# Performance work log

Measured on AMD Instinct MI355X. Metric: run time of the kernel, lower is better.

## Reference

```python
import jax, jax.numpy as jnp
import numpy as np

LEN_M = 131328   # (data_dim+1) * d_h = 513 * 256
D_H = 256
N_MC = 64
DATA_DIM_P1 = 513
N = 4096


def setup_inputs() -> dict:
    key = jax.random.key(0)
    k1, k2, k3, k4 = jax.random.split(key, 4)
    params = jax.random.normal(k1, (2 * LEN_M,), dtype=jnp.float32)
    W1 = jax.random.normal(k2, (D_H + 1,), dtype=jnp.float32)
    x = jax.random.normal(k3, (N, DATA_DIM_P1), dtype=jnp.float32)
    eps = jax.random.normal(k4, (N_MC,), dtype=jnp.float32)
    return {"params": params, "W1": W1, "x": x, "eps": eps}


def reference(params, W1, x, eps):
    # split variational params into means and (relu'd) variances
    m_w0 = params[:LEN_M]                                  # [len_m]
    v_w0 = jax.nn.relu(params[LEN_M:]) + 1e-6              # [len_m]
    # reparameterized MC sampling; NOTE: torch code draws ONE scalar eps per
    # MC sample (randn(m_w0[0].shape) is scalar), shared across all weights.
    samps_w0 = m_w0[:, None] + eps[None, :] * jnp.sqrt(v_w0)[:, None]  # [len_m, M]
    W0 = samps_w0.reshape(DATA_DIM_P1, D_H, N_MC)          # [d+1, h, M]
    # fused batched GEMM replacing the d_h * num_MC_samps tiny matmuls
    x_w0 = jnp.einsum('nd,dhm->nhm', x, W0)                # [N, h, M]
    z = jax.nn.relu(x_w0)
    ones = jnp.ones((x.shape[0], 1, N_MC), dtype=x.dtype)
    z = jnp.concatenate([ones, z], axis=1)                 # [N, h+1, M]
    pred_samps = jnp.einsum('nhm,h->nm', z, W1)            # [N, M]
    return pred_samps, m_w0, v_w0
```

## Files before the change

kernel.cpp:

```cpp
#include <hip/hip_runtime.h>
#include <hip/hip_bf16.h>
#include <math.h>

#define LEN_M   131328
#define D_P1    513
#define NROW    4096
#define PRED_ELEMS (NROW * 64)

typedef __attribute__((ext_vector_type(8))) short short8;
typedef __attribute__((ext_vector_type(4))) float floatx4;
typedef __attribute__((ext_vector_type(2))) float v2f;

__device__ __forceinline__ void gl_lds16(const void* g, void* l)
{
    __builtin_amdgcn_global_load_lds(
        (const __attribute__((address_space(1))) unsigned int*)g,
        (__attribute__((address_space(3))) unsigned int*)l, 16, 0, 0);
}

__device__ __forceinline__ unsigned short bf16b(float f)
{
    __hip_bfloat16 h = __float2bfloat16(f);
    return *(unsigned short*)&h;
}

__global__ __launch_bounds__(256) void prep_kernel(
    const float* __restrict__ params, float* __restrict__ out,
    __hip_bfloat16* __restrict__ wcbt)
{
    __shared__ unsigned short T[64][65];
    const int bid = blockIdx.x;
    const int t   = threadIdx.x;

    if (bid < 1024) {
        int i = bid * 256 + t;
        out[i] = 0.0f;
        if (i < LEN_M) {
            float m = params[i];
            float v = fmaxf(params[LEN_M + i], 0.0f) + 1e-6f;
            out[PRED_ELEMS + i]         = m;
            out[PRED_ELEMS + LEN_M + i] = v;
        }
        return;
    }

    const int b2 = bid - 1024;
    const int k0 = (b2 & 7) * 64;
    const int c0 = (b2 >> 3) * 64;
    const int hh = t & 63, kb = t >> 6;
    const bool spart = (c0 >= 256);
    const int hbase = c0 & 255;
    const float* src = params + (spart ? LEN_M : 0);

    #pragma unroll 4
    for (int p = 0; p < 16; ++p) {
        int kk = p * 4 + kb;
        float v = src[(k0 + kk) * 256 + hbase + hh];
        if (spart) v = sqrtf(fmaxf(v, 0.0f) + 1e-6f);
        T[kk][hh] = bf16b(v);
    }
    __syncthreads();

    const int cc = t >> 2, kq = t & 3;
    short8 lo, hi;
    #pragma unroll
    for (int j = 0; j < 8; ++j) lo[j] = (short)T[kq * 16 + j][cc];
    #pragma unroll
    for (int j = 0; j < 8; ++j) hi[j] = (short)T[kq * 16 + 8 + j][cc];

    const int cR  = c0 + cc;
    const int swz = (cR >> 1) & 3;
    const int g1  = (k0 >> 3) + 2 * kq;
    const int g2  = g1 + 1;
    const int d1  = cR * 64 + (g1 & ~3) + ((g1 & 3) ^ swz);
    const int d2  = cR * 64 + (g2 & ~3) + ((g2 & 3) ^ swz);
    short* wb = (short*)wcbt;
    *(short8*)(wb + d1 * 8) = lo;
    *(short8*)(wb + d2 * 8) = hi;
}

__global__ __launch_bounds__(256) void main_kernel(
    const __hip_bfloat16* __restrict__ wcbt, const float* __restrict__ params,
    const float* __restrict__ x, const float* __restrict__ W1,
    const float* __restrict__ eps, float* __restrict__ out)
{
    __shared__ char smem[128 * 36 * 4];
    short* Bs   = (short*)smem;
    short* As   = (short*)(smem + 8192);
    float* Clds = (float*)smem;

    const int t = threadIdx.x;
    const int w4 = t >> 6, lane = t & 63;
    const int lane15 = lane & 15, quad = lane >> 4;
    const int H  = blockIdx.x;
    const int bm = blockIdx.y * 32;

    const short* wb = (const short*)wcbt;
    const short* bsrc0; const short* bsrc1; short* bdst0; short* bdst1;
    {
        int ch0 = t, ch1 = 256 + t;
        int lc0 = ch0 >> 2, qs0 = ch0 & 3;
        int lc1 = ch1 >> 2, qs1 = ch1 & 3;
        int c0g = H * 64 + lc0 + ((lc0 >> 6) * 192);
        int c1g = H * 64 + lc1 + ((lc1 >> 6) * 192);
        bsrc0 = wb + (c0g * 64 + qs0) * 8;
        bsrc1 = wb + (c1g * 64 + qs1) * 8;
        bdst0 = Bs + ch0 * 8;
        bdst1 = Bs + ch1 * 8;
    }

    const int ar = t >> 3, asub = t & 7;
    const int aq = asub >> 1, ahalf = asub & 1;
    const float* axp = x + (bm + ar) * D_P1 + asub * 4;
    unsigned short* adst = (unsigned short*)As + ar * 32
                         + ((aq ^ ((ar >> 1) & 3)) * 8) + ahalf * 4;

    const float e = eps[lane];
    float xl[2][4];
    #pragma unroll
    for (int rh = 0; rh < 2; ++rh)
        #pragma unroll
        for (int i = 0; i < 4; ++i)
            xl[rh][i] = x[(bm + rh * 16 + quad * 4 + i) * D_P1 + 512];
    float wl[2];
    #pragma unroll
    for (int s = 0; s < 2; ++s) {
        int lc = w4 * 32 + s * 16 + lane15;
        int c  = H * 64 + lc + ((lc >> 6) * 192);
        wl[s] = (c < 256) ? params[131072 + c]
                          : sqrtf(fmaxf(params[LEN_M + 131072 + (c - 256)], 0.0f) + 1e-6f);
    }

    const short* afp[2]; const short* bfp[2];
    #pragma unroll
    for (int rh = 0; rh < 2; ++rh) {
        int row = rh * 16 + lane15;
        afp[rh] = As + row * 32 + ((quad ^ ((row >> 1) & 3)) * 8);
    }
    #pragma unroll
    for (int s = 0; s < 2; ++s) {
        int lc = w4 * 32 + s * 16 + lane15;
        bfp[s] = Bs + lc * 32 + ((quad ^ ((lc >> 1) & 3)) * 8);
    }

    floatx4 acc00 = {0.f,0.f,0.f,0.f}, acc01 = acc00, acc10 = acc00, acc11 = acc00;

    for (int ks = 0; ks < 16; ++ks) {
        gl_lds16(bsrc0 + ks * 32, bdst0);
        gl_lds16(bsrc1 + ks * 32, bdst1);
        float f0 = axp[ks * 32 + 0], f1 = axp[ks * 32 + 1];
        float f2 = axp[ks * 32 + 2], f3 = axp[ks * 32 + 3];
        ushort4 pk;
        pk.x = bf16b(f0); pk.y = bf16b(f1); pk.z = bf16b(f2); pk.w = bf16b(f3);
        *(ushort4*)adst = pk;
        __syncthreads();

        short8 a0 = *(const short8*)afp[0];
        short8 a1 = *(const short8*)afp[1];
        short8 b0 = *(const short8*)bfp[0];
        short8 b1 = *(const short8*)bfp[1];
        acc00 = __builtin_amdgcn_mfma_f32_16x16x32_bf16(a0, b0, acc00, 0, 0, 0);
        acc01 = __builtin_amdgcn_mfma_f32_16x16x32_bf16(a0, b1, acc01, 0, 0, 0);
        acc10 = __builtin_amdgcn_mfma_f32_16x16x32_bf16(a1, b0, acc10, 0, 0, 0);
        acc11 = __builtin_amdgcn_mfma_f32_16x16x32_bf16(a1, b1, acc11, 0, 0, 0);
        __syncthreads();
    }

    floatx4 accs[2][2] = {{acc00, acc01}, {acc10, acc11}};
    #pragma unroll
    for (int rh = 0; rh < 2; ++rh)
        #pragma unroll
        for (int s = 0; s < 2; ++s) {
            float4 o;
            o.x = accs[rh][s][0] + xl[rh][0] * wl[s];
            o.y = accs[rh][s][1] + xl[rh][1] * wl[s];
            o.z = accs[rh][s][2] + xl[rh][2] * wl[s];
            o.w = accs[rh][s][3] + xl[rh][3] * wl[s];
            int lc = w4 * 32 + s * 16 + lane15;
            int r0 = rh * 16 + quad * 4;
            *(float4*)&Clds[lc * 36 + r0] = o;
        }
    __syncthreads();

    const int rb = w4 * 8;
    const float binit = (H == 0) ? W1[0] : 0.0f;
    v2f accp[4];
    #pragma unroll
    for (int j = 0; j < 4; ++j) accp[j] = (v2f){binit, binit};
    const v2f e2 = {e, e};
    const v2f z2 = {0.f, 0.f};

    #pragma unroll 4
    for (int lh = 0; lh < 64; ++lh) {
        const float w1h = W1[1 + H * 64 + lh];
        const v2f w2 = {w1h, w1h};
        const v2f* ap = (const v2f*)&Clds[lh * 36 + rb];
        const v2f* bp = (const v2f*)&Clds[(64 + lh) * 36 + rb];
        #pragma unroll
        for (int j = 0; j < 4; ++j) {
            v2f t2 = __builtin_elementwise_fma(e2, bp[j], ap[j]);
            t2 = __builtin_elementwise_max(t2, z2);
            accp[j] = __builtin_elementwise_fma(t2, w2, accp[j]);
        }
    }

    float* op = out + (bm + rb) * 64 + lane;
    #pragma unroll
    for (int j = 0; j < 4; ++j) {
        unsafeAtomicAdd(op + (2 * j) * 64,     accp[j].x);
        unsafeAtomicAdd(op + (2 * j + 1) * 64, accp[j].y);
    }
}

extern "C" void kernel_launch(void* const* d_in, const int* in_sizes, int n_in,
                              void* d_out, int out_size, void* d_ws, size_t ws_size,
                              hipStream_t stream)
{
    const float* params = (const float*)d_in[0];
    const float* W1     = (const float*)d_in[1];
    const float* x      = (const float*)d_in[2];
    const float* eps    = (const float*)d_in[3];
    float* out = (float*)d_out;
    __hip_bfloat16* wcbt = (__hip_bfloat16*)d_ws;

    prep_kernel<<<1024 + 64, 256, 0, stream>>>(params, out, wcbt);
    main_kernel<<<dim3(4, 128), 256, 0, stream>>>(wcbt, params, x, W1, eps, out);
}
```

Before: 85.21 us.

## Stage full A tile in LDS upfront and double-buffer B loads

The main kernel now converts and stores the whole 32x512 bf16 A tile into LDS once before the K loop, using a new XOR swizzle. It also double-buffers the B tile so the global-to-LDS load for the next K step is issued while the current step's MFMAs run. This drops one barrier per iteration and overlaps global latency with compute. In exchange LDS use grows to 48 KB, and the last iteration prefetches one step past the tile, reading into the next column or possibly past the workspace end.

Result: no change. 84.83 us (-0.5%).

```diff
diff --git a/kernel.cpp b/kernel.cpp
--- a/kernel.cpp
+++ b/kernel.cpp
@@ -84,10 +84,10 @@
     const float* __restrict__ x, const float* __restrict__ W1,
     const float* __restrict__ eps, float* __restrict__ out)
 {
-    __shared__ char smem[128 * 36 * 4];
-    short* Bs   = (short*)smem;
-    short* As   = (short*)(smem + 8192);
-    float* Clds = (float*)smem;
+    __shared__ char smem[49152];
+    char*  Bs   = smem;
+    char*  As   = smem + 16384;
+    float* Clds = (float*)(smem + 16384);
 
     const int t = threadIdx.x;
     const int w4 = t >> 6, lane = t & 63;
@@ -96,7 +96,7 @@
     const int bm = blockIdx.y * 32;
 
     const short* wb = (const short*)wcbt;
-    const short* bsrc0; const short* bsrc1; short* bdst0; short* bdst1;
+    const short* bsrc0; const short* bsrc1;
     {
         int ch0 = t, ch1 = 256 + t;
         int lc0 = ch0 >> 2, qs0 = ch0 & 3;
@@ -105,15 +105,29 @@
         int c1g = H * 64 + lc1 + ((lc1 >> 6) * 192);
         bsrc0 = wb + (c0g * 64 + qs0) * 8;
         bsrc1 = wb + (c1g * 64 + qs1) * 8;
-        bdst0 = Bs + ch0 * 8;
-        bdst1 = Bs + ch1 * 8;
-    }
-
-    const int ar = t >> 3, asub = t & 7;
-    const int aq = asub >> 1, ahalf = asub & 1;
-    const float* axp = x + (bm + ar) * D_P1 + asub * 4;
-    unsigned short* adst = (unsigned short*)As + ar * 32
-                         + ((aq ^ ((ar >> 1) & 3)) * 8) + ahalf * 4;
+    }
+    char* bd0 = Bs + t * 16;
+    char* bd1 = Bs + 4096 + t * 16;
+
+    gl_lds16(bsrc0, bd0);
+    gl_lds16(bsrc1, bd1);
+
+    {
+        const int ar = t >> 3, a8 = t & 7;
+        const float* axp = x + (bm + ar) * D_P1;
+        unsigned short* arow = (unsigned short*)As + ar * 512;
+        #pragma unroll 4
+        for (int ks = 0; ks < 16; ++ks) {
+            int k = ks * 32 + a8 * 4;
+            float f0 = axp[k], f1 = axp[k + 1], f2 = axp[k + 2], f3 = axp[k + 3];
+            int chunk = k >> 3;
+            int half  = a8 & 1;
+            int cs = (chunk & ~7) | ((chunk & 7) ^ (ar & 7));
+            ushort4 pk;
+            pk.x = bf16b(f0); pk.y = bf16b(f1); pk.z = bf16b(f2); pk.w = bf16b(f3);
+            *(ushort4*)(arow + cs * 8 + half * 4) = pk;
+        }
+    }
 
     const float e = eps[lane];
     float xl[2][4];
@@ -131,34 +145,30 @@
                           : sqrtf(fmaxf(params[LEN_M + 131072 + (c - 256)], 0.0f) + 1e-6f);
     }
 
-    const short* afp[2]; const short* bfp[2];
-    #pragma unroll
-    for (int rh = 0; rh < 2; ++rh) {
-        int row = rh * 16 + lane15;
-        afp[rh] = As + row * 32 + ((quad ^ ((row >> 1) & 3)) * 8);
-    }
+    int bfo[2];
     #pragma unroll
     for (int s = 0; s < 2; ++s) {
         int lc = w4 * 32 + s * 16 + lane15;
-        bfp[s] = Bs + lc * 32 + ((quad ^ ((lc >> 1) & 3)) * 8);
-    }
+        bfo[s] = lc * 64 + ((quad ^ ((lc >> 1) & 3)) * 16);
+    }
+    const int ax7 = lane15 & 7;
 
     floatx4 acc00 = {0.f,0.f,0.f,0.f}, acc01 = acc00, acc10 = acc00, acc11 = acc00;
 
+    __syncthreads();
+
     for (int ks = 0; ks < 16; ++ks) {
-        gl_lds16(bsrc0 + ks * 32, bdst0);
-        gl_lds16(bsrc1 + ks * 32, bdst1);
-        float f0 = axp[ks * 32 + 0], f1 = axp[ks * 32 + 1];
-        float f2 = axp[ks * 32 + 2], f3 = axp[ks * 32 + 3];
-        ushort4 pk;
-        pk.x = bf16b(f0); pk.y = bf16b(f1); pk.z = bf16b(f2); pk.w = bf16b(f3);
-        *(ushort4*)adst = pk;
-        __syncthreads();
-
-        short8 a0 = *(const short8*)afp[0];
-        short8 a1 = *(const short8*)afp[1];
-        short8 b0 = *(const short8*)bfp[0];
-        short8 b1 = *(const short8*)bfp[1];
+        const int nb = (ks + 1) & 1;
+        gl_lds16(bsrc0 + (ks + 1) * 32, bd0 + nb * 8192);
+        gl_lds16(bsrc1 + (ks + 1) * 32, bd1 + nb * 8192);
+
+        const int cs16 = ((ks >> 1) * 8 + (((ks & 1) * 4 + quad) ^ ax7)) * 16;
+        short8 a0 = *(const short8*)(As + lane15 * 1024 + cs16);
+        short8 a1 = *(const short8*)(As + (16 + lane15) * 1024 + cs16);
+        const char* Bb = Bs + (ks & 1) * 8192;
+        short8 b0 = *(const short8*)(Bb + bfo[0]);
+        short8 b1 = *(const short8*)(Bb + bfo[1]);
+
         acc00 = __builtin_amdgcn_mfma_f32_16x16x32_bf16(a0, b0, acc00, 0, 0, 0);
         acc01 = __builtin_amdgcn_mfma_f32_16x16x32_bf16(a0, b1, acc01, 0, 0, 0);
         acc10 = __builtin_amdgcn_mfma_f32_16x16x32_bf16(a1, b0, acc10, 0, 0, 0);
```

## Restructure main GEMM to full-width 512-column tiles with double-buffered LDS

Applied to the files above, without the earlier changes.

Each block now owns 16 rows and all 512 weight columns (means and std parts), so the ReLU/W1 reduction finishes inside the block. This removes the atomic adds and the zeroing of the prediction output. The weight workspace layout changes to k-chunk-major with an XOR swizzle, so whole 64-deep k-chunks stream into LDS through double buffering. The bf16 row of x is converted once up front. The cost is 144KB of dynamic LDS per block, which limits occupancy to one block per CU with only 256 blocks.

New measurement: 84.43 us. No clear change (-0.9%).

```diff
diff --git a/kernel.cpp b/kernel.cpp
--- a/kernel.cpp
+++ b/kernel.cpp
@@ -32,19 +32,16 @@
     const int bid = blockIdx.x;
     const int t   = threadIdx.x;
 
-    if (bid < 1024) {
+    if (bid < 513) {
         int i = bid * 256 + t;
-        out[i] = 0.0f;
-        if (i < LEN_M) {
-            float m = params[i];
-            float v = fmaxf(params[LEN_M + i], 0.0f) + 1e-6f;
-            out[PRED_ELEMS + i]         = m;
-            out[PRED_ELEMS + LEN_M + i] = v;
-        }
+        float m = params[i];
+        float v = fmaxf(params[LEN_M + i], 0.0f) + 1e-6f;
+        out[PRED_ELEMS + i]         = m;
+        out[PRED_ELEMS + LEN_M + i] = v;
         return;
     }
 
-    const int b2 = bid - 1024;
+    const int b2 = bid - 513;
     const int k0 = (b2 & 7) * 64;
     const int c0 = (b2 >> 3) * 64;
     const int hh = t & 63, kb = t >> 6;
@@ -68,147 +65,148 @@
     #pragma unroll
     for (int j = 0; j < 8; ++j) hi[j] = (short)T[kq * 16 + 8 + j][cc];
 
-    const int cR  = c0 + cc;
-    const int swz = (cR >> 1) & 3;
-    const int g1  = (k0 >> 3) + 2 * kq;
-    const int g2  = g1 + 1;
-    const int d1  = cR * 64 + (g1 & ~3) + ((g1 & 3) ^ swz);
-    const int d2  = cR * 64 + (g2 & ~3) + ((g2 & 3) ^ swz);
+    const int cR = c0 + cc;
+    const int g1 = (k0 >> 3) + 2 * kq;
+    const int g2 = g1 + 1;
+    const int d1 = (g1 >> 3) * 4096 + cR * 8 + ((g1 & 7) ^ (cR & 7));
+    const int d2 = (g2 >> 3) * 4096 + cR * 8 + ((g2 & 7) ^ (cR & 7));
     short* wb = (short*)wcbt;
     *(short8*)(wb + d1 * 8) = lo;
     *(short8*)(wb + d2 * 8) = hi;
 }
 
-__global__ __launch_bounds__(256) void main_kernel(
+__global__ __launch_bounds__(512) void main_kernel(
     const __hip_bfloat16* __restrict__ wcbt, const float* __restrict__ params,
     const float* __restrict__ x, const float* __restrict__ W1,
     const float* __restrict__ eps, float* __restrict__ out)
 {
-    __shared__ char smem[128 * 36 * 4];
-    short* Bs   = (short*)smem;
-    short* As   = (short*)(smem + 8192);
-    float* Clds = (float*)smem;
+    extern __shared__ char smem[];
+    char*  Ap = smem + 131072;
+    float* Cl = (float*)smem;
+    float* P  = (float*)(smem + 40960);
 
     const int t = threadIdx.x;
-    const int w4 = t >> 6, lane = t & 63;
+    const int w = t >> 6, lane = t & 63;
     const int lane15 = lane & 15, quad = lane >> 4;
-    const int H  = blockIdx.x;
-    const int bm = blockIdx.y * 32;
-
-    const short* wb = (const short*)wcbt;
-    const short* bsrc0; const short* bsrc1; short* bdst0; short* bdst1;
+    const int ax7 = lane15 & 7;
+    const int bm = blockIdx.x * 16;
+
+    const char* wbase = (const char*)wcbt;
+
+    #pragma unroll
+    for (int i = 0; i < 8; ++i)
+        gl_lds16(wbase + (0 * 4096 + i * 512 + t) * 16, smem + i * 8192 + t * 16);
+
     {
-        int ch0 = t, ch1 = 256 + t;
-        int lc0 = ch0 >> 2, qs0 = ch0 & 3;
-        int lc1 = ch1 >> 2, qs1 = ch1 & 3;
-        int c0g = H * 64 + lc0 + ((lc0 >> 6) * 192);
-        int c1g = H * 64 + lc1 + ((lc1 >> 6) * 192);
-        bsrc0 = wb + (c0g * 64 + qs0) * 8;
-        bsrc1 = wb + (c1g * 64 + qs1) * 8;
-        bdst0 = Bs + ch0 * 8;
-        bdst1 = Bs + ch1 * 8;
-    }
-
-    const int ar = t >> 3, asub = t & 7;
-    const int aq = asub >> 1, ahalf = asub & 1;
-    const float* axp = x + (bm + ar) * D_P1 + asub * 4;
-    unsigned short* adst = (unsigned short*)As + ar * 32
-                         + ((aq ^ ((ar >> 1) & 3)) * 8) + ahalf * 4;
+        const int r = t >> 5, seg = t & 31;
+        const float* xrow = x + (bm + r) * D_P1 + seg * 16;
+        #pragma unroll
+        for (int c2 = 0; c2 < 2; ++c2) {
+            int g  = seg * 2 + c2;
+            int cs = (g & ~7) | ((g & 7) ^ (r & 7));
+            short8 pk;
+            #pragma unroll
+            for (int j = 0; j < 8; ++j) pk[j] = (short)bf16b(xrow[c2 * 8 + j]);
+            *(short8*)(Ap + r * 1024 + cs * 16) = pk;
+        }
+    }
 
     const float e = eps[lane];
-    float xl[2][4];
-    #pragma unroll
-    for (int rh = 0; rh < 2; ++rh)
-        #pragma unroll
-        for (int i = 0; i < 4; ++i)
-            xl[rh][i] = x[(bm + rh * 16 + quad * 4 + i) * D_P1 + 512];
-    float wl[2];
-    #pragma unroll
-    for (int s = 0; s < 2; ++s) {
-        int lc = w4 * 32 + s * 16 + lane15;
-        int c  = H * 64 + lc + ((lc >> 6) * 192);
+    float xl[4];
+    #pragma unroll
+    for (int i = 0; i < 4; ++i)
+        xl[i] = x[(bm + quad * 4 + i) * D_P1 + 512];
+    float wl[4];
+    #pragma unroll
+    for (int s = 0; s < 4; ++s) {
+        int c = (s < 2 ? 0 : 256) + w * 32 + (s & 1) * 16 + lane15;
         wl[s] = (c < 256) ? params[131072 + c]
                           : sqrtf(fmaxf(params[LEN_M + 131072 + (c - 256)], 0.0f) + 1e-6f);
     }
 
-    const short* afp[2]; const short* bfp[2];
-    #pragma unroll
-    for (int rh = 0; rh < 2; ++rh) {
-        int row = rh * 16 + lane15;
-        afp[rh] = As + row * 32 + ((quad ^ ((row >> 1) & 3)) * 8);
-    }
-    #pragma unroll
-    for (int s = 0; s < 2; ++s) {
-        int lc = w4 * 32 + s * 16 + lane15;
-        bfp[s] = Bs + lc * 32 + ((quad ^ ((lc >> 1) & 3)) * 8);
-    }
-
-    floatx4 acc00 = {0.f,0.f,0.f,0.f}, acc01 = acc00, acc10 = acc00, acc11 = acc00;
-
-    for (int ks = 0; ks < 16; ++ks) {
-        gl_lds16(bsrc0 + ks * 32, bdst0);
-        gl_lds16(bsrc1 + ks * 32, bdst1);
-        float f0 = axp[ks * 32 + 0], f1 = axp[ks * 32 + 1];
-        float f2 = axp[ks * 32 + 2], f3 = axp[ks * 32 + 3];
-        ushort4 pk;
-        pk.x = bf16b(f0); pk.y = bf16b(f1); pk.z = bf16b(f2); pk.w = bf16b(f3);
-        *(ushort4*)adst = pk;
+    int cb[4];
+    #pragma unroll
+    for (int s = 0; s < 4; ++s)
+        cb[s] = ((s < 2 ? 0 : 256) + w * 32 + (s & 1) * 16 + lane15) * 128;
+
+    floatx4 acc[4];
+    #pragma unroll
+    for (int s = 0; s < 4; ++s) acc[s] = (floatx4){0.f, 0.f, 0.f, 0.f};
+
+    __syncthreads();
+
+    for (int kc = 0; kc < 8; ++kc) {
+        if (kc < 7) {
+            const int nb = (kc + 1) & 1;
+            #pragma unroll
+            for (int i = 0; i < 8; ++i)
+                gl_lds16(wbase + ((kc + 1) * 4096 + i * 512 + t) * 16,
+                         smem + nb * 65536 + i * 8192 + t * 16);
+        }
+        const char* Bb = smem + (kc & 1) * 65536;
+        const char* Ab = Ap + lane15 * 1024 + kc * 128;
+        #pragma unroll
+        for (int kk = 0; kk < 2; ++kk) {
+            const int off = ((kk * 4 + quad) ^ ax7) * 16;
+            short8 a  = *(const short8*)(Ab + off);
+            short8 b0 = *(const short8*)(Bb + cb[0] + off);
+            short8 b1 = *(const short8*)(Bb + cb[1] + off);
+            short8 b2 = *(const short8*)(Bb + cb[2] + off);
+            short8 b3 = *(const short8*)(Bb + cb[3] + off);
+            acc[0] = __builtin_amdgcn_mfma_f32_16x16x32_bf16(a, b0, acc[0], 0, 0, 0);
+            acc[1] = __builtin_amdgcn_mfma_f32_16x16x32_bf16(a, b1, acc[1], 0, 0, 0);
+            acc[2] = __builtin_amdgcn_mfma_f32_16x16x32_bf16(a, b2, acc[2], 0, 0, 0);
+            acc[3] = __builtin_amdgcn_mfma_f32_16x16x32_bf16(a, b3, acc[3], 0, 0, 0);
+        }
         __syncthreads();
-
-        short8 a0 = *(const short8*)afp[0];
-        short8 a1 = *(const short8*)afp[1];
-        short8 b0 = *(const short8*)bfp[0];
-        short8 b1 = *(const short8*)bfp[1];
-        acc00 = __builtin_amdgcn_mfma_f32_16x16x32_bf16(a0, b0, acc00, 0, 0, 0);
-        acc01 = __builtin_amdgcn_mfma_f32_16x16x32_bf16(a0, b1, acc01, 0, 0, 0);
-        acc10 = __builtin_amdgcn_mfma_f32_16x16x32_bf16(a1, b0, acc10, 0, 0, 0);
-        acc11 = __builtin_amdgcn_mfma_f32_16x16x32_bf16(a1, b1, acc11, 0, 0, 0);
-        __syncthreads();
-    }
-
-    floatx4 accs[2][2] = {{acc00, acc01}, {acc10, acc11}};
-    #pragma unroll
-    for (int rh = 0; rh < 2; ++rh)
-        #pragma unroll
-        for (int s = 0; s < 2; ++s) {
-            float4 o;
-            o.x = accs[rh][s][0] + xl[rh][0] * wl[s];
-            o.y = accs[rh][s][1] + xl[rh][1] * wl[s];
-            o.z = accs[rh][s][2] + xl[rh][2] * wl[s];
-            o.w = accs[rh][s][3] + xl[rh][3] * wl[s];
-            int lc = w4 * 32 + s * 16 + lane15;
-            int r0 = rh * 16 + quad * 4;
-            *(float4*)&Clds[lc * 36 + r0] = o;
-        }
-    __syncthreads();
-
-    const int rb = w4 * 8;
-    const float binit = (H == 0) ? W1[0] : 0.0f;
-    v2f accp[4];
-    #pragma unroll
-    for (int j = 0; j < 4; ++j) accp[j] = (v2f){binit, binit};
-    const v2f e2 = {e, e};
-    const v2f z2 = {0.f, 0.f};
+    }
+
+    #pragma unroll
+    for (int s = 0; s < 4; ++s) {
+        int gc = (s < 2 ? 0 : 256) + w * 32 + (s & 1) * 16 + lane15;
+        float4 o;
+        o.x = acc[s][0] + xl[0] * wl[s];
+        o.y = acc[s][1] + xl[1] * wl[s];
+        o.z = acc[s][2] + xl[2] * wl[s];
+        o.w = acc[s][3] + xl[3] * wl[s];
+        *(float4*)&Cl[gc * 20 + quad * 4] = o;
+    }
+    __syncthreads();
+
+    const int rq = (w & 3) * 4;
+    const int hb = (w >> 2) * 128;
+    v2f a01s = {0.f, 0.f}, a23s = {0.f, 0.f};
+    const v2f e2 = {e, e}, z2 = {0.f, 0.f};
 
     #pragma unroll 4
-    for (int lh = 0; lh < 64; ++lh) {
-        const float w1h = W1[1 + H * 64 + lh];
+    for (int hh = 0; hh < 128; ++hh) {
+        const int h = hb + hh;
+        const float w1h = W1[1 + h];
         const v2f w2 = {w1h, w1h};
-        const v2f* ap = (const v2f*)&Clds[lh * 36 + rb];
-        const v2f* bp = (const v2f*)&Clds[(64 + lh) * 36 + rb];
-        #pragma unroll
-        for (int j = 0; j < 4; ++j) {
-            v2f t2 = __builtin_elementwise_fma(e2, bp[j], ap[j]);
-            t2 = __builtin_elementwise_max(t2, z2);
-            accp[j] = __builtin_elementwise_fma(t2, w2, accp[j]);
-        }
-    }
-
-    float* op = out + (bm + rb) * 64 + lane;
-    #pragma unroll
-    for (int j = 0; j < 4; ++j) {
-        unsafeAtomicAdd(op + (2 * j) * 64,     accp[j].x);
-        unsafeAtomicAdd(op + (2 * j + 1) * 64, accp[j].y);
+        const float4 av = *(const float4*)&Cl[h * 20 + rq];
+        const float4 bv = *(const float4*)&Cl[(256 + h) * 20 + rq];
+        v2f a01 = {av.x, av.y}, a23 = {av.z, av.w};
+        v2f b01 = {bv.x, bv.y}, b23 = {bv.z, bv.w};
+        v2f t01 = __builtin_elementwise_max(__builtin_elementwise_fma(e2, b01, a01), z2);
+        v2f t23 = __builtin_elementwise_max(__builtin_elementwise_fma(e2, b23, a23), z2);
+        a01s = __builtin_elementwise_fma(t01, w2, a01s);
+        a23s = __builtin_elementwise_fma(t23, w2, a23s);
+    }
+
+    if (w >= 4) {
+        float* p = P + (w - 4) * 256 + lane;
+        p[0]   = a01s.x; p[64]  = a01s.y;
+        p[128] = a23s.x; p[192] = a23s.y;
+    }
+    __syncthreads();
+    if (w < 4) {
+        const float b0 = W1[0];
+        const float* p = P + w * 256 + lane;
+        float* op = out + (bm + rq) * 64 + lane;
+        op[0]   = a01s.x + p[0]   + b0;
+        op[64]  = a01s.y + p[64]  + b0;
+        op[128] = a23s.x + p[128] + b0;
+        op[192] = a23s.y + p[192] + b0;
     }
 }
 
@@ -223,6 +221,13 @@
     float* out = (float*)d_out;
     __hip_bfloat16* wcbt = (__hip_bfloat16*)d_ws;
 
-    prep_kernel<<<1024 + 64, 256, 0, stream>>>(params, out, wcbt);
-    main_kernel<<<dim3(4, 128), 256, 0, stream>>>(wcbt, params, x, W1, eps, out);
-}
+    static bool attr_set = false;
+    if (!attr_set) {
+        hipFuncSetAttribute((const void*)main_kernel,
+                            hipFuncAttributeMaxDynamicSharedMemorySize, 147456);
+        attr_set = true;
+    }
+
+    prep_kernel<<<513 + 64, 256, 0, stream>>>(params, out, wcbt);
+    main_kernel<<<256, 512, 147456, stream>>>(wcbt, params, x, W1, eps, out);
+}
```
